# Performance work log

Measured on AMD Instinct MI355X. Metric: run time of the kernel, lower is better.

The kernel has to match this reference:

```python
import jax, jax.numpy as jnp
import numpy as np

B, N, D = 8, 8192, 256
NPOINT, NSAMPLE, WNET = 2048, 32, 16
IN_CH = D + 3
OUT_CH = 512
LEAKY = 0.1


def setup_inputs() -> dict:
    key = jax.random.key(0)
    ks = jax.random.split(key, 8)
    def p(k, shape, s=0.1):
        return jax.random.normal(k, shape, jnp.float32) * s
    return {
        "xyz": jax.random.normal(ks[0], (B, 3, N), jnp.float32),
        "points": jax.random.normal(ks[1], (B, D, N), jnp.float32),
        "w1": p(ks[2], (8, 3)), "b1": jnp.zeros((8,), jnp.float32),
        "w2": p(ks[3], (8, 8)), "b2": jnp.zeros((8,), jnp.float32),
        "w3": p(ks[4], (WNET, 8)), "b3": jnp.zeros((WNET,), jnp.float32),
        "lin_w": p(ks[5], (OUT_CH, WNET * IN_CH), 0.02),
        "lin_b": jnp.zeros((OUT_CH,), jnp.float32),
    }


def fps(xyz_t, npoint):
    # furthest point sampling; xyz_t: [B,N,3] -> idx [B,npoint] (first idx = 0)
    b, n, _ = xyz_t.shape
    def body(i, carry):
        idx, dists, last = carry
        centroid = jnp.take_along_axis(xyz_t, last[:, None, None], axis=1)  # [B,1,3]
        d = jnp.sum((xyz_t - centroid) ** 2, axis=-1)                        # [B,N]
        dists = jnp.minimum(dists, d)
        nxt = jnp.argmax(dists, axis=-1).astype(jnp.int32)                   # [B]
        return idx.at[:, i].set(nxt), dists, nxt
    idx0 = jnp.zeros((b, npoint), jnp.int32)
    last0 = jnp.zeros((b,), jnp.int32)
    d0 = jnp.full((b, n), 1e10, xyz_t.dtype)
    idx, _, _ = jax.lax.fori_loop(1, npoint, body, (idx0, d0, last0))
    return idx


def knn(nsample, xyz_t, new_xyz):
    # squared pairwise dists [B,S,N]; k smallest -> neighbor indices [B,S,K]
    d = (jnp.sum(new_xyz ** 2, -1)[:, :, None]
         + jnp.sum(xyz_t ** 2, -1)[:, None, :]
         - 2.0 * jnp.einsum('bsc,bnc->bsn', new_xyz, xyz_t))
    _, idx = jax.lax.top_k(-d, nsample)
    return idx


def gather(pts, idx):
    # pts [B,N,C], idx [B,S,K] -> [B,S,K,C]
    return jax.vmap(lambda p, i: p[i])(pts, idx)


def reference(xyz, points, w1, b1, w2, b2, w3, b3, lin_w, lin_b):
    xyz_t = xyz.transpose(0, 2, 1)      # [B,N,3]
    pts_t = points.transpose(0, 2, 1)   # [B,N,D]
    fps_idx = fps(xyz_t, NPOINT)
    new_xyz = jnp.take_along_axis(xyz_t, fps_idx[:, :, None], axis=1)  # [B,S,3]
    idx = knn(NSAMPLE, xyz_t, new_xyz)
    grouped_xyz_norm = gather(xyz_t, idx) - new_xyz[:, :, None, :]     # [B,S,K,3]
    new_points = jnp.concatenate([grouped_xyz_norm, gather(pts_t, idx)], axis=-1)  # [B,S,K,3+D]
    # WeightNet: 1x1-conv MLP 3 -> 8 -> 8 -> WNET, ReLU after each layer (bn=False)
    h = jax.nn.relu(grouped_xyz_norm @ w1.T + b1)
    h = jax.nn.relu(h @ w2.T + b2)
    w = jax.nn.relu(h @ w3.T + b3)                                     # [B,S,K,WNET]
    # per-point weighted aggregation: [B,S,C,K] @ [B,S,K,WNET] -> [B,S,C*WNET]
    agg = jnp.einsum('bskc,bskw->bscw', new_points, w).reshape(xyz.shape[0], NPOINT, -1)
    out = agg @ lin_w.T + lin_b                                        # [B,S,OUT_CH]
    out = out.transpose(0, 2, 1)                                       # [B,OUT_CH,S]
    out = jnp.where(out > 0, out, LEAKY * out)                         # LeakyReLU(0.1)
    return new_xyz.transpose(0, 2, 1), out, fps_idx
```

## Files before the change

### kernel.cpp

```cpp
#include <hip/hip_runtime.h>

#define NB 8
#define NN 8192
#define ND 256
#define NPOINT 2048
#define NSAMPLE 32
#define WNET 16
#define INCH 259
#define OUTCH 512
#define KPAD 4160

typedef short short8 __attribute__((ext_vector_type(8)));
typedef float float4v __attribute__((ext_vector_type(4)));
typedef unsigned long long u64;

__device__ __forceinline__ unsigned short f2bf(float x){
  unsigned u = __float_as_uint(x);
  u = (u + 0x7FFFu + ((u >> 16) & 1u)) >> 16;
  return (unsigned short)u;
}
__device__ __forceinline__ float bf2f(unsigned short v){
  return __uint_as_float(((unsigned)v) << 16);
}

__device__ __forceinline__ u64 wave_max_dpp(u64 k){
#define DPPSTEP(ctrl) {                                                        \
    unsigned lo = (unsigned)k, hi = (unsigned)(k >> 32);                       \
    unsigned olo = (unsigned)__builtin_amdgcn_update_dpp(0, (int)lo, ctrl, 0xf, 0xf, true); \
    unsigned ohi = (unsigned)__builtin_amdgcn_update_dpp(0, (int)hi, ctrl, 0xf, 0xf, true); \
    u64 o = (((u64)ohi) << 32) | olo;                                          \
    if (o > k) k = o; }
  DPPSTEP(0x111)
  DPPSTEP(0x112)
  DPPSTEP(0x114)
  DPPSTEP(0x118)
  DPPSTEP(0x142)
  DPPSTEP(0x143)
#undef DPPSTEP
  return k;
}

__device__ __forceinline__ u64 row16_max_dpp(u64 k){
#define DPPSTEP(ctrl) {                                                        \
    unsigned lo = (unsigned)k, hi = (unsigned)(k >> 32);                       \
    unsigned olo = (unsigned)__builtin_amdgcn_update_dpp(0, (int)lo, ctrl, 0xf, 0xf, true); \
    unsigned ohi = (unsigned)__builtin_amdgcn_update_dpp(0, (int)hi, ctrl, 0xf, 0xf, true); \
    u64 o = (((u64)ohi) << 32) | olo;                                          \
    if (o > k) k = o; }
  DPPSTEP(0x111)
  DPPSTEP(0x112)
  DPPSTEP(0x114)
  DPPSTEP(0x118)
#undef DPPSTEP
  return k;
}

__device__ __forceinline__ unsigned p1b2(unsigned v){
  v &= 0x3FFu;
  v = (v | (v << 16)) & 0x030000FFu;
  v = (v | (v << 8))  & 0x0300F00Fu;
  v = (v | (v << 4))  & 0x030C30C3u;
  v = (v | (v << 2))  & 0x09249249u;
  return v;
}

__global__ __launch_bounds__(1024) void morton_sort_kernel(
    const float* __restrict__ xyz, float* __restrict__ sx, float* __restrict__ sy,
    float* __restrict__ sz, int* __restrict__ sorig){
  __shared__ u64 arr[NN];
  const int b = blockIdx.x, t = threadIdx.x;
  const float* xp = xyz + (size_t)b * 3 * NN;
#pragma unroll
  for (int j = 0; j < 8; j++){
    int n = t + j * 1024;
    float x = xp[n], y = xp[NN + n], z = xp[2 * NN + n];
    unsigned qx = (unsigned)fminf(1023.f, fmaxf(0.f, (x + 6.f) * 85.25f));
    unsigned qy = (unsigned)fminf(1023.f, fmaxf(0.f, (y + 6.f) * 85.25f));
    unsigned qz = (unsigned)fminf(1023.f, fmaxf(0.f, (z + 6.f) * 85.25f));
    unsigned key = (p1b2(qz) << 2) | (p1b2(qy) << 1) | p1b2(qx);
    arr[n] = (((u64)key) << 13) | (unsigned)n;
  }
  __syncthreads();
  for (int k = 2; k <= NN; k <<= 1){
    for (int j = k >> 1; j >= 1; j >>= 1){
#pragma unroll
      for (int pi = 0; pi < 4; pi++){
        int p = t + pi * 1024;
        int lo = ((p & ~(j - 1)) << 1) | (p & (j - 1));
        int hi = lo | j;
        bool asc = (lo & k) == 0;
        u64 a = arr[lo], c = arr[hi];
        if (asc ? (a > c) : (c > a)){ arr[lo] = c; arr[hi] = a; }
      }
      __syncthreads();
    }
  }
#pragma unroll
  for (int j = 0; j < 8; j++){
    int n = t + j * 1024;
    int orig = (int)(arr[n] & 8191u);
    sx[(size_t)b * NN + n] = xp[orig];
    sy[(size_t)b * NN + n] = xp[NN + orig];
    sz[(size_t)b * NN + n] = xp[2 * NN + orig];
    sorig[(size_t)b * NN + n] = orig;
  }
}

__global__ __launch_bounds__(1024) void fps_kernel(
    const float* __restrict__ sxg, const float* __restrict__ syg,
    const float* __restrict__ szg, const int* __restrict__ sorigg,
    float* __restrict__ out0, float* __restrict__ out2, float* __restrict__ wnew){
#pragma clang fp contract(off)
  __shared__ float4v pxyz[NN];
  __shared__ u64 seq[NPOINT];
  __shared__ u64 red[2][16];
  __shared__ int s_pos0;
  const int b = blockIdx.x, t = threadIdx.x;
  const int lane = t & 63, w = t >> 6;
  const int base = w * 512 + lane * 8;
  const float* gx = sxg + (size_t)b * NN;
  const float* gy = syg + (size_t)b * NN;
  const float* gz = szg + (size_t)b * NN;
  const int*   go = sorigg + (size_t)b * NN;

  float x[8], y[8], z[8], ld[8]; int so[8];
#pragma unroll
  for (int j = 0; j < 8; j++){
    int n = base + j;
    x[j] = gx[n]; y[j] = gy[n]; z[j] = gz[n]; so[j] = go[n];
    pxyz[n] = (float4v){x[j], y[j], z[j], 0.f};
    if (so[j] == 0) s_pos0 = n;
    ld[j] = 1e10f;
  }
  float mnx = x[0], mxx = x[0], mny = y[0], mxy = y[0], mnz = z[0], mxz = z[0];
#pragma unroll
  for (int j = 1; j < 8; j++){
    mnx = fminf(mnx, x[j]); mxx = fmaxf(mxx, x[j]);
    mny = fminf(mny, y[j]); mxy = fmaxf(mxy, y[j]);
    mnz = fminf(mnz, z[j]); mxz = fmaxf(mxz, z[j]);
  }
  const float ccx = (mnx + mxx) * 0.5f, ccy = (mny + mxy) * 0.5f, ccz = (mnz + mxz) * 0.5f;
  float R2 = 0.f;
#pragma unroll
  for (int j = 0; j < 8; j++){
    float dx = x[j] - ccx, dy = y[j] - ccy, dz = z[j] - ccz;
    R2 = fmaxf(R2, (dx * dx + dy * dy) + dz * dz);
  }
  const float R = sqrtf(R2) * 1.001f + 1e-7f;
  float thr = 3e38f;
  u64 wkey = 0;
  __syncthreads();

  int pos = s_pos0;
  float4v c4 = pxyz[pos];
  float cx = c4[0], cy = c4[1], cz = c4[2];
  if (t == 0) seq[0] = (((u64)8191) << 13) | (unsigned)pos;

  for (int i = 1; i < NPOINT; i++){
    float qdx = cx - ccx, qdy = cy - ccy, qdz = cz - ccz;
    float q = (qdx * qdx + qdy * qdy) + qdz * qdz;
    if (__any(q < thr)){
      float bv = -1.f; int bo = 0, bp = 0;
#pragma unroll
      for (int j = 0; j < 8; j++){
        float dx = x[j] - cx, dy = y[j] - cy, dz = z[j] - cz;
        float d  = (dx * dx + dy * dy) + dz * dz;
        float nd = fminf(ld[j], d);
        ld[j] = nd;
        bool better = (nd > bv) || (nd == bv && so[j] < bo);
        bv = better ? nd : bv;
        bo = better ? so[j] : bo;
        bp = better ? (base + j) : bp;
      }
      float sr = sqrtf(bv) * 1.001f + R;
      thr = sr * sr;
      u64 k2 = (((u64)__float_as_uint(bv)) << 26) | (((u64)(8191 - bo)) << 13) | (unsigned)bp;
      wkey = wave_max_dpp(k2);
    }
    if (lane == 63) red[i & 1][w] = wkey;
    __syncthreads();
    u64 rv = red[i & 1][lane & 15];
    rv = row16_max_dpp(rv);
    unsigned rlo = (unsigned)__builtin_amdgcn_readlane((int)(unsigned)rv, 15);
    unsigned rhi = (unsigned)__builtin_amdgcn_readlane((int)(unsigned)(rv >> 32), 15);
    u64 v = (((u64)rhi) << 32) | rlo;
    pos = (int)(v & 8191u);
    float4v n4 = pxyz[pos];
    cx = n4[0]; cy = n4[1]; cz = n4[2];
    if (t == 0) seq[i] = v;
  }
  __syncthreads();
  for (int k = t; k < NPOINT; k += 1024){
    u64 v = seq[k];
    int p = (int)(v & 8191u);
    int orig = 8191 - (int)((v >> 13) & 8191u);
    float4v pv = pxyz[p];
    out2[b * NPOINT + k] = (float)orig;
    out0[(size_t)b * 3 * NPOINT + k]              = pv[0];
    out0[(size_t)b * 3 * NPOINT + NPOINT + k]     = pv[1];
    out0[(size_t)b * 3 * NPOINT + 2 * NPOINT + k] = pv[2];
    float* wp = wnew + ((size_t)b * NPOINT + k) * 3;
    wp[0] = pv[0]; wp[1] = pv[1]; wp[2] = pv[2];
  }
}

__global__ __launch_bounds__(1024) void transpose_points(
    const float* __restrict__ pts, unsigned short* __restrict__ ptsT){
  __shared__ float tile[64][65];
  const int b  = blockIdx.z;
  const int n0 = blockIdx.x * 64;
  const int d0 = blockIdx.y * 64;
  const int tx = threadIdx.x, ty = threadIdx.y;
  const float* src = pts + ((size_t)b * ND + d0) * NN + n0;
#pragma unroll
  for (int j = 0; j < 4; j++){
    int d = ty + j * 16;
    tile[d][tx] = src[(size_t)d * NN + tx];
  }
  __syncthreads();
  unsigned short* dst = ptsT + ((size_t)b * NN + n0) * ND + d0;
#pragma unroll
  for (int j = 0; j < 4; j++){
    int n = ty + j * 16;
    dst[(size_t)n * ND + tx] = f2bf(tile[tx][n]);
  }
}

__global__ __launch_bounds__(256) void convert_linw(
    const float* __restrict__ lw, unsigned short* __restrict__ out){
  int i = blockIdx.x * 256 + threadIdx.x;
  if (i >= OUTCH * KPAD) return;
  int o = i / KPAD, f = i - o * KPAD;
  float v = (f < WNET * INCH) ? lw[(size_t)o * (WNET * INCH) + f] : 0.f;
  out[i] = f2bf(v);
}

__device__ __forceinline__ void find_bin64(const unsigned* hist, unsigned r,
                                           unsigned* outB, unsigned* outC, int lane){
  unsigned h0 = hist[lane * 4 + 0], h1 = hist[lane * 4 + 1];
  unsigned h2 = hist[lane * 4 + 2], h3 = hist[lane * 4 + 3];
  unsigned s4 = h0 + h1 + h2 + h3;
  unsigned sc = s4;
#pragma unroll
  for (int off = 1; off < 64; off <<= 1){
    unsigned o = __shfl_up(sc, off, 64);
    if (lane >= off) sc += o;
  }
  unsigned cum = sc - s4;
  if (cum < r && cum + h0 >= r){ *outB = lane * 4 + 0; *outC = cum; } cum += h0;
  if (cum < r && cum + h1 >= r){ *outB = lane * 4 + 1; *outC = cum; } cum += h1;
  if (cum < r && cum + h2 >= r){ *outB = lane * 4 + 2; *outC = cum; } cum += h2;
  if (cum < r && cum + h3 >= r){ *outB = lane * 4 + 3; *outC = cum; } cum += h3;
}

__global__ __launch_bounds__(256) void knn_kernel(const float* __restrict__ xyz,
    const float* __restrict__ newxyz, int* __restrict__ ws_idx){
  __shared__ unsigned key[NN];
  __shared__ unsigned hist[256];
  __shared__ int s_sel[48];
  __shared__ unsigned candk[256];
  __shared__ int candi[256];
  __shared__ int s_selcnt, s_candcnt;
  __shared__ unsigned s_info[4];
  const int q = blockIdx.x;
  const int b = q >> 11;
  const int t = threadIdx.x;
  const float* xp = xyz + (size_t)b * 3 * NN;
  float qx = newxyz[q * 3], qy = newxyz[q * 3 + 1], qz = newxyz[q * 3 + 2];
  float qq = qx * qx + qy * qy + qz * qz;
#pragma unroll 4
  for (int j = 0; j < 32; j++){
    int n = t + j * 256;
    float px = xp[n], py = xp[NN + n], pz = xp[2 * NN + n];
    float pp = px * px + py * py + pz * pz;
    float d  = qq + pp - 2.f * (qx * px + qy * py + qz * pz);
    unsigned u = __float_as_uint(d);
    u ^= (u & 0x80000000u) ? 0xFFFFFFFFu : 0x80000000u;
    key[n] = u;
  }
  hist[t] = 0;
  if (t == 0){ s_selcnt = 0; s_candcnt = 0; }
  __syncthreads();
#pragma unroll 4
  for (int j = 0; j < 32; j++){
    int n = t + j * 256;
    atomicAdd(&hist[key[n] >> 24], 1u);
  }
  __syncthreads();
  if (t < 64) find_bin64(hist, NSAMPLE, &s_info[0], &s_info[1], t);
  __syncthreads();
  unsigned B1 = s_info[0], c0 = s_info[1];
  hist[t] = 0;
  __syncthreads();
#pragma unroll 4
  for (int j = 0; j < 32; j++){
    int n = t + j * 256;
    unsigned u = key[n];
    if ((u >> 24) == B1) atomicAdd(&hist[(u >> 16) & 0xFFu], 1u);
  }
  __syncthreads();
  if (t < 64) find_bin64(hist, NSAMPLE - c0, &s_info[2], &s_info[3], t);
  __syncthreads();
  unsigned T16 = (B1 << 8) | s_info[2];
  int c01 = (int)(c0 + s_info[3]);
#pragma unroll 4
  for (int j = 0; j < 32; j++){
    int n = t + j * 256;
    unsigned k16 = key[n] >> 16;
    if (k16 < T16){
      int p = atomicAdd(&s_selcnt, 1);
      s_sel[p] = n;
    } else if (k16 == T16){
      int p = atomicAdd(&s_candcnt, 1);
      if (p < 256){ candk[p] = key[n]; candi[p] = n; }
    }
  }
  __syncthreads();
  const int m = NSAMPLE - c01;
  const int L = s_candcnt;
  if (t < 64){
    u64 prev = 0;
    for (int r = 0; r < m; r++){
      u64 best = ~0ULL;
      if (L <= 256){
        for (int j = t; j < L; j += 64){
          u64 pk = (((u64)candk[j]) << 32) | (unsigned)candi[j];
          if (pk > prev && pk < best) best = pk;
        }
      } else {
        for (int j = 0; j < 128; j++){
          int n = t + j * 64;
          unsigned u = key[n];
          if ((u >> 16) == T16){
            u64 pk = (((u64)u) << 32) | (unsigned)n;
            if (pk > prev && pk < best) best = pk;
          }
        }
      }
#pragma unroll
      for (int off = 32; off > 0; off >>= 1){
        u64 o = __shfl_down(best, off, 64);
        if (o < best) best = o;
      }
      best = __shfl(best, 0, 64);
      if (t == 0) s_sel[c01 + r] = (int)(best & 0xFFFFFFFFu);
      prev = best;
    }
  }
  __syncthreads();
  if (t < NSAMPLE) ws_idx[(size_t)q * NSAMPLE + t] = s_sel[t];
}

__global__ __launch_bounds__(256) void agg_kernel(
    const float* __restrict__ xyz, const float* __restrict__ newxyz,
    const int* __restrict__ ws_idx, const unsigned short* __restrict__ ptsT,
    const float* __restrict__ w1, const float* __restrict__ b1,
    const float* __restrict__ w2, const float* __restrict__ b2,
    const float* __restrict__ w3, const float* __restrict__ b3,
    unsigned short* __restrict__ agg){
  __shared__ float feat[32][257];
  __shared__ float __align__(16) wgt[32][16];
  __shared__ float xyzn[32][4];
  __shared__ int nid[32];
  const int q = blockIdx.x;
  const int b = q >> 11;
  const int t = threadIdx.x;
  if (t < 32) nid[t] = ws_idx[(size_t)q * NSAMPLE + t];
  __syncthreads();
  if (t < 32){
    int n = nid[t];
    const float* xp = xyz + (size_t)b * 3 * NN;
    float qx = newxyz[q * 3], qy = newxyz[q * 3 + 1], qz = newxyz[q * 3 + 2];
    float xn = xp[n] - qx, yn = xp[NN + n] - qy, zn = xp[2 * NN + n] - qz;
    xyzn[t][0] = xn; xyzn[t][1] = yn; xyzn[t][2] = zn;
    float h1[8], h2[8];
#pragma unroll
    for (int i = 0; i < 8; i++)
      h1[i] = fmaxf(0.f, w1[i * 3] * xn + w1[i * 3 + 1] * yn + w1[i * 3 + 2] * zn + b1[i]);
#pragma unroll
    for (int i = 0; i < 8; i++){
      float a = b2[i];
#pragma unroll
      for (int j = 0; j < 8; j++) a += w2[i * 8 + j] * h1[j];
      h2[i] = fmaxf(0.f, a);
    }
#pragma unroll
    for (int i = 0; i < 16; i++){
      float a = b3[i];
#pragma unroll
      for (int j = 0; j < 8; j++) a += w3[i * 8 + j] * h2[j];
      wgt[t][i] = fmaxf(0.f, a);
    }
  }
#pragma unroll
  for (int j = 0; j < 4; j++){
    int c = t + 256 * j;
    int row = c >> 5, col = c & 31;
    const uint4* src = (const uint4*)(ptsT + ((size_t)b * NN + nid[row]) * ND) + col;
    uint4 v = *src;
    float* dstf = &feat[row][col * 8];
    dstf[0] = bf2f((unsigned short)(v.x & 0xFFFF)); dstf[1] = bf2f((unsigned short)(v.x >> 16));
    dstf[2] = bf2f((unsigned short)(v.y & 0xFFFF)); dstf[3] = bf2f((unsigned short)(v.y >> 16));
    dstf[4] = bf2f((unsigned short)(v.z & 0xFFFF)); dstf[5] = bf2f((unsigned short)(v.z >> 16));
    dstf[6] = bf2f((unsigned short)(v.w & 0xFFFF)); dstf[7] = bf2f((unsigned short)(v.w >> 16));
  }
  __syncthreads();
  for (int c = t; c < INCH; c += 256){
    const float* npb; int stride;
    if (c < 3){ npb = &xyzn[0][c]; stride = 4; }
    else      { npb = &feat[0][c - 3]; stride = 257; }
    float acc[16];
#pragma unroll
    for (int i = 0; i < 16; i++) acc[i] = 0.f;
    for (int k = 0; k < 32; k++){
      float v = npb[k * stride];
      const float4v* wr = (const float4v*)(&wgt[k][0]);
      float4v a0 = wr[0], a1 = wr[1], a2 = wr[2], a3 = wr[3];
      acc[0]  += v * a0[0]; acc[1]  += v * a0[1]; acc[2]  += v * a0[2]; acc[3]  += v * a0[3];
      acc[4]  += v * a1[0]; acc[5]  += v * a1[1]; acc[6]  += v * a1[2]; acc[7]  += v * a1[3];
      acc[8]  += v * a2[0]; acc[9]  += v * a2[1]; acc[10] += v * a2[2]; acc[11] += v * a2[3];
      acc[12] += v * a3[0]; acc[13] += v * a3[1]; acc[14] += v * a3[2]; acc[15] += v * a3[3];
    }
    unsigned r[8];
#pragma unroll
    for (int p = 0; p < 8; p++)
      r[p] = (unsigned)f2bf(acc[2 * p]) | ((unsigned)f2bf(acc[2 * p + 1]) << 16);
    uint4* dst = (uint4*)(agg + (size_t)q * KPAD + c * WNET);
    uint4 v0 = {r[0], r[1], r[2], r[3]};
    uint4 v1 = {r[4], r[5], r[6], r[7]};
    dst[0] = v0; dst[1] = v1;
  }
  if (t == 3){
    uint4 z = {0, 0, 0, 0};
    uint4* dst = (uint4*)(agg + (size_t)q * KPAD + WNET * INCH);
    dst[0] = z; dst[1] = z;
  }
}

#define BM 128
#define BN 128
#define BK 64
__global__ __launch_bounds__(256) void gemm_kernel(
    const unsigned short* __restrict__ A, const unsigned short* __restrict__ W,
    const float* __restrict__ bias, float* __restrict__ out1){
  __shared__ short __align__(16) As[BM * BK];
  __shared__ short __align__(16) Ws[BN * BK];
  const int t = threadIdx.x;
  const int m0 = blockIdx.x * BM;
  const int n0 = blockIdx.y * BN;
  const int wave = t >> 6, lane = t & 63;
  const int wm = (wave >> 1) * 64, wn = (wave & 1) * 64;
  const int lrow = lane & 15, quad = lane >> 4;
  float4v acc[4][4];
#pragma unroll
  for (int i = 0; i < 4; i++)
#pragma unroll
    for (int j = 0; j < 4; j++) acc[i][j] = (float4v){0.f, 0.f, 0.f, 0.f};

  for (int k0 = 0; k0 < KPAD; k0 += BK){
#pragma unroll
    for (int j = 0; j < 4; j++){
      int chunk = t + 256 * j;
      int row = chunk >> 3, c = chunk & 7;
      uint4 v = *(const uint4*)(A + (size_t)(m0 + row) * KPAD + k0 + c * 8);
      *(uint4*)&As[chunk * 8] = v;
    }
#pragma unroll
    for (int j = 0; j < 4; j++){
      int chunk = t + 256 * j;
      int row = chunk >> 3, c = chunk & 7;
      uint4 v = *(const uint4*)(W + (size_t)(n0 + row) * KPAD + k0 + c * 8);
      *(uint4*)&Ws[chunk * 8] = v;
    }
    __syncthreads();
#pragma unroll
    for (int kk = 0; kk < 2; kk++){
      short8 a[4], w[4];
      int kof = kk * 32 + quad * 8;
#pragma unroll
      for (int i = 0; i < 4; i++){
        a[i] = *(const short8*)&As[(wm + i * 16 + lrow) * BK + kof];
        w[i] = *(const short8*)&Ws[(wn + i * 16 + lrow) * BK + kof];
      }
#pragma unroll
      for (int i = 0; i < 4; i++)
#pragma unroll
        for (int j = 0; j < 4; j++)
          acc[i][j] = __builtin_amdgcn_mfma_f32_16x16x32_bf16(a[i], w[j], acc[i][j], 0, 0, 0);
    }
    __syncthreads();
  }
#pragma unroll
  for (int i = 0; i < 4; i++){
#pragma unroll
    for (int j = 0; j < 4; j++){
      int m = m0 + wm + i * 16 + quad * 4;
      int n = n0 + wn + j * 16 + lrow;
      float bv = bias[n];
      int bb = m >> 11, s = m & 2047;
      float* dst = out1 + ((size_t)bb * OUTCH + n) * NPOINT + s;
      float4v v = acc[i][j];
      float4v r;
#pragma unroll
      for (int e = 0; e < 4; e++){
        float x = v[e] + bv;
        r[e] = x > 0.f ? x : 0.1f * x;
      }
      *(float4v*)dst = r;
    }
  }
}

extern "C" void kernel_launch(void* const* d_in, const int* in_sizes, int n_in,
                              void* d_out, int out_size, void* d_ws, size_t ws_size,
                              hipStream_t stream) {
  const float* xyz    = (const float*)d_in[0];
  const float* points = (const float*)d_in[1];
  const float* w1 = (const float*)d_in[2];
  const float* b1 = (const float*)d_in[3];
  const float* w2 = (const float*)d_in[4];
  const float* b2 = (const float*)d_in[5];
  const float* w3 = (const float*)d_in[6];
  const float* b3 = (const float*)d_in[7];
  const float* lin_w = (const float*)d_in[8];
  const float* lin_b = (const float*)d_in[9];

  float* out0 = (float*)d_out;
  float* out1 = out0 + (size_t)NB * 3 * NPOINT;
  float* out2 = out1 + (size_t)NB * OUTCH * NPOINT;

  char* ws = (char*)d_ws;
  float* ws_newxyz = (float*)ws;                                   size_t o = (size_t)NB * NPOINT * 3 * 4;
  int* ws_idx = (int*)(ws + o);                                    o += (size_t)NB * NPOINT * NSAMPLE * 4;
  unsigned short* ws_ptsT = (unsigned short*)(ws + o);             o += (size_t)NB * NN * ND * 2;
  unsigned short* ws_lw = (unsigned short*)(ws + o);               o += (size_t)OUTCH * KPAD * 2;
  unsigned short* ws_agg = (unsigned short*)(ws + o);              o += (size_t)NB * NPOINT * KPAD * 2;
  float* ws_sx = (float*)(ws + o);                                 o += (size_t)NB * NN * 4;
  float* ws_sy = (float*)(ws + o);                                 o += (size_t)NB * NN * 4;
  float* ws_sz = (float*)(ws + o);                                 o += (size_t)NB * NN * 4;
  int*   ws_so = (int*)(ws + o);                                   o += (size_t)NB * NN * 4;

  morton_sort_kernel<<<NB, 1024, 0, stream>>>(xyz, ws_sx, ws_sy, ws_sz, ws_so);
  fps_kernel<<<NB, 1024, 0, stream>>>(ws_sx, ws_sy, ws_sz, ws_so, out0, out2, ws_newxyz);
  transpose_points<<<dim3(NN / 64, ND / 64, NB), dim3(64, 16), 0, stream>>>(points, ws_ptsT);
  convert_linw<<<(OUTCH * KPAD + 255) / 256, 256, 0, stream>>>(lin_w, ws_lw);
  knn_kernel<<<NB * NPOINT, 256, 0, stream>>>(xyz, ws_newxyz, ws_idx);
  agg_kernel<<<NB * NPOINT, 256, 0, stream>>>(xyz, ws_newxyz, ws_idx, ws_ptsT,
                                              w1, b1, w2, b2, w3, b3, ws_agg);
  gemm_kernel<<<dim3(NB * NPOINT / BM, OUTCH / BN), 256, 0, stream>>>(ws_agg, ws_lw, lin_b, out1);
}
```

Baseline: 3.751 ms.

## Fuse FPS with KNN+aggregation in a persistent kernel overlapping via progress flags

Merges the morton sort, point transpose and weight conversion into one prep launch. A persistent mega kernel then runs FPS on 8 blocks while the other blocks pull query indices from a global atomic counter. Each worker spins on per-batch FPS progress counters so KNN and aggregation for already-emitted centroids overlap with the serial FPS loop. KNN and aggregation are fused in one block, so the neighbor index buffer is no longer written and read back. The risks are spin-wait correctness, the 248-block launch needing all blocks co-resident, and large LDS use per block.

Result: faster. 3.039 ms (-19.0%).

```diff
diff --git a/kernel.cpp b/kernel.cpp
--- a/kernel.cpp
+++ b/kernel.cpp
@@ -40,21 +40,6 @@
   return k;
 }
 
-__device__ __forceinline__ u64 row16_max_dpp(u64 k){
-#define DPPSTEP(ctrl) {                                                        \
-    unsigned lo = (unsigned)k, hi = (unsigned)(k >> 32);                       \
-    unsigned olo = (unsigned)__builtin_amdgcn_update_dpp(0, (int)lo, ctrl, 0xf, 0xf, true); \
-    unsigned ohi = (unsigned)__builtin_amdgcn_update_dpp(0, (int)hi, ctrl, 0xf, 0xf, true); \
-    u64 o = (((u64)ohi) << 32) | olo;                                          \
-    if (o > k) k = o; }
-  DPPSTEP(0x111)
-  DPPSTEP(0x112)
-  DPPSTEP(0x114)
-  DPPSTEP(0x118)
-#undef DPPSTEP
-  return k;
-}
-
 __device__ __forceinline__ unsigned p1b2(unsigned v){
   v &= 0x3FFu;
   v = (v | (v << 16)) & 0x030000FFu;
@@ -64,175 +49,83 @@
   return v;
 }
 
-__global__ __launch_bounds__(1024) void morton_sort_kernel(
-    const float* __restrict__ xyz, float* __restrict__ sx, float* __restrict__ sy,
-    float* __restrict__ sz, int* __restrict__ sorig){
-  __shared__ u64 arr[NN];
-  const int b = blockIdx.x, t = threadIdx.x;
-  const float* xp = xyz + (size_t)b * 3 * NN;
-#pragma unroll
-  for (int j = 0; j < 8; j++){
-    int n = t + j * 1024;
-    float x = xp[n], y = xp[NN + n], z = xp[2 * NN + n];
-    unsigned qx = (unsigned)fminf(1023.f, fmaxf(0.f, (x + 6.f) * 85.25f));
-    unsigned qy = (unsigned)fminf(1023.f, fmaxf(0.f, (y + 6.f) * 85.25f));
-    unsigned qz = (unsigned)fminf(1023.f, fmaxf(0.f, (z + 6.f) * 85.25f));
-    unsigned key = (p1b2(qz) << 2) | (p1b2(qy) << 1) | p1b2(qx);
-    arr[n] = (((u64)key) << 13) | (unsigned)n;
+#define TRB 4096
+#define CVB 2080
+__global__ __launch_bounds__(1024) void prep_kernel(
+    const float* __restrict__ xyz, const float* __restrict__ pts,
+    const float* __restrict__ lw,
+    float* __restrict__ sx, float* __restrict__ sy, float* __restrict__ sz,
+    int* __restrict__ sorig, unsigned short* __restrict__ ptsT,
+    unsigned short* __restrict__ lwout, unsigned* __restrict__ psync){
+  __shared__ __align__(16) char smem[65536];
+  const int bid = blockIdx.x, t = threadIdx.x;
+  if (bid < NB){
+    u64* arr = (u64*)smem;
+    const int b = bid;
+    if (t == 0){ psync[b] = 0; if (b == 0) psync[8] = 0; }
+    const float* xp = xyz + (size_t)b * 3 * NN;
+#pragma unroll
+    for (int j = 0; j < 8; j++){
+      int n = t + j * 1024;
+      float x = xp[n], y = xp[NN + n], z = xp[2 * NN + n];
+      unsigned qx = (unsigned)fminf(1023.f, fmaxf(0.f, (x + 6.f) * 85.25f));
+      unsigned qy = (unsigned)fminf(1023.f, fmaxf(0.f, (y + 6.f) * 85.25f));
+      unsigned qz = (unsigned)fminf(1023.f, fmaxf(0.f, (z + 6.f) * 85.25f));
+      unsigned key = (p1b2(qz) << 2) | (p1b2(qy) << 1) | p1b2(qx);
+      arr[n] = (((u64)key) << 13) | (unsigned)n;
+    }
+    __syncthreads();
+    for (int k = 2; k <= NN; k <<= 1){
+      for (int j = k >> 1; j >= 1; j >>= 1){
+#pragma unroll
+        for (int pi = 0; pi < 4; pi++){
+          int p = t + pi * 1024;
+          int lo = ((p & ~(j - 1)) << 1) | (p & (j - 1));
+          int hi = lo | j;
+          bool asc = (lo & k) == 0;
+          u64 a = arr[lo], c = arr[hi];
+          if (asc ? (a > c) : (c > a)){ arr[lo] = c; arr[hi] = a; }
+        }
+        __syncthreads();
+      }
+    }
+#pragma unroll
+    for (int j = 0; j < 8; j++){
+      int n = t + j * 1024;
+      int orig = (int)(arr[n] & 8191u);
+      sx[(size_t)b * NN + n] = xp[orig];
+      sy[(size_t)b * NN + n] = xp[NN + orig];
+      sz[(size_t)b * NN + n] = xp[2 * NN + orig];
+      sorig[(size_t)b * NN + n] = orig;
+    }
+  } else if (bid < NB + TRB){
+    float (*tile)[65] = (float(*)[65])smem;
+    const int r = bid - NB;
+    const int n0 = (r & 127) * 64;
+    const int d0 = ((r >> 7) & 3) * 64;
+    const int b  = r >> 9;
+    const int tx = t & 63, ty = t >> 6;
+    const float* src = pts + ((size_t)b * ND + d0) * NN + n0;
+#pragma unroll
+    for (int j = 0; j < 4; j++){
+      int d = ty + j * 16;
+      tile[d][tx] = src[(size_t)d * NN + tx];
+    }
+    __syncthreads();
+    unsigned short* dst = ptsT + ((size_t)b * NN + n0) * ND + d0;
+#pragma unroll
+    for (int j = 0; j < 4; j++){
+      int n = ty + j * 16;
+      dst[(size_t)n * ND + tx] = f2bf(tile[tx][n]);
+    }
+  } else {
+    int i = (bid - NB - TRB) * 1024 + t;
+    if (i < OUTCH * KPAD){
+      int o = i / KPAD, f = i - o * KPAD;
+      float v = (f < WNET * INCH) ? lw[(size_t)o * (WNET * INCH) + f] : 0.f;
+      lwout[i] = f2bf(v);
+    }
   }
-  __syncthreads();
-  for (int k = 2; k <= NN; k <<= 1){
-    for (int j = k >> 1; j >= 1; j >>= 1){
-#pragma unroll
-      for (int pi = 0; pi < 4; pi++){
-        int p = t + pi * 1024;
-        int lo = ((p & ~(j - 1)) << 1) | (p & (j - 1));
-        int hi = lo | j;
-        bool asc = (lo & k) == 0;
-        u64 a = arr[lo], c = arr[hi];
-        if (asc ? (a > c) : (c > a)){ arr[lo] = c; arr[hi] = a; }
-      }
-      __syncthreads();
-    }
-  }
-#pragma unroll
-  for (int j = 0; j < 8; j++){
-    int n = t + j * 1024;
-    int orig = (int)(arr[n] & 8191u);
-    sx[(size_t)b * NN + n] = xp[orig];
-    sy[(size_t)b * NN + n] = xp[NN + orig];
-    sz[(size_t)b * NN + n] = xp[2 * NN + orig];
-    sorig[(size_t)b * NN + n] = orig;
-  }
-}
-
-__global__ __launch_bounds__(1024) void fps_kernel(
-    const float* __restrict__ sxg, const float* __restrict__ syg,
-    const float* __restrict__ szg, const int* __restrict__ sorigg,
-    float* __restrict__ out0, float* __restrict__ out2, float* __restrict__ wnew){
-#pragma clang fp contract(off)
-  __shared__ float4v pxyz[NN];
-  __shared__ u64 seq[NPOINT];
-  __shared__ u64 red[2][16];
-  __shared__ int s_pos0;
-  const int b = blockIdx.x, t = threadIdx.x;
-  const int lane = t & 63, w = t >> 6;
-  const int base = w * 512 + lane * 8;
-  const float* gx = sxg + (size_t)b * NN;
-  const float* gy = syg + (size_t)b * NN;
-  const float* gz = szg + (size_t)b * NN;
-  const int*   go = sorigg + (size_t)b * NN;
-
-  float x[8], y[8], z[8], ld[8]; int so[8];
-#pragma unroll
-  for (int j = 0; j < 8; j++){
-    int n = base + j;
-    x[j] = gx[n]; y[j] = gy[n]; z[j] = gz[n]; so[j] = go[n];
-    pxyz[n] = (float4v){x[j], y[j], z[j], 0.f};
-    if (so[j] == 0) s_pos0 = n;
-    ld[j] = 1e10f;
-  }
-  float mnx = x[0], mxx = x[0], mny = y[0], mxy = y[0], mnz = z[0], mxz = z[0];
-#pragma unroll
-  for (int j = 1; j < 8; j++){
-    mnx = fminf(mnx, x[j]); mxx = fmaxf(mxx, x[j]);
-    mny = fminf(mny, y[j]); mxy = fmaxf(mxy, y[j]);
-    mnz = fminf(mnz, z[j]); mxz = fmaxf(mxz, z[j]);
-  }
-  const float ccx = (mnx + mxx) * 0.5f, ccy = (mny + mxy) * 0.5f, ccz = (mnz + mxz) * 0.5f;
-  float R2 = 0.f;
-#pragma unroll
-  for (int j = 0; j < 8; j++){
-    float dx = x[j] - ccx, dy = y[j] - ccy, dz = z[j] - ccz;
-    R2 = fmaxf(R2, (dx * dx + dy * dy) + dz * dz);
-  }
-  const float R = sqrtf(R2) * 1.001f + 1e-7f;
-  float thr = 3e38f;
-  u64 wkey = 0;
-  __syncthreads();
-
-  int pos = s_pos0;
-  float4v c4 = pxyz[pos];
-  float cx = c4[0], cy = c4[1], cz = c4[2];
-  if (t == 0) seq[0] = (((u64)8191) << 13) | (unsigned)pos;
-
-  for (int i = 1; i < NPOINT; i++){
-    float qdx = cx - ccx, qdy = cy - ccy, qdz = cz - ccz;
-    float q = (qdx * qdx + qdy * qdy) + qdz * qdz;
-    if (__any(q < thr)){
-      float bv = -1.f; int bo = 0, bp = 0;
-#pragma unroll
-      for (int j = 0; j < 8; j++){
-        float dx = x[j] - cx, dy = y[j] - cy, dz = z[j] - cz;
-        float d  = (dx * dx + dy * dy) + dz * dz;
-        float nd = fminf(ld[j], d);
-        ld[j] = nd;
-        bool better = (nd > bv) || (nd == bv && so[j] < bo);
-        bv = better ? nd : bv;
-        bo = better ? so[j] : bo;
-        bp = better ? (base + j) : bp;
-      }
-      float sr = sqrtf(bv) * 1.001f + R;
-      thr = sr * sr;
-      u64 k2 = (((u64)__float_as_uint(bv)) << 26) | (((u64)(8191 - bo)) << 13) | (unsigned)bp;
-      wkey = wave_max_dpp(k2);
-    }
-    if (lane == 63) red[i & 1][w] = wkey;
-    __syncthreads();
-    u64 rv = red[i & 1][lane & 15];
-    rv = row16_max_dpp(rv);
-    unsigned rlo = (unsigned)__builtin_amdgcn_readlane((int)(unsigned)rv, 15);
-    unsigned rhi = (unsigned)__builtin_amdgcn_readlane((int)(unsigned)(rv >> 32), 15);
-    u64 v = (((u64)rhi) << 32) | rlo;
-    pos = (int)(v & 8191u);
-    float4v n4 = pxyz[pos];
-    cx = n4[0]; cy = n4[1]; cz = n4[2];
-    if (t == 0) seq[i] = v;
-  }
-  __syncthreads();
-  for (int k = t; k < NPOINT; k += 1024){
-    u64 v = seq[k];
-    int p = (int)(v & 8191u);
-    int orig = 8191 - (int)((v >> 13) & 8191u);
-    float4v pv = pxyz[p];
-    out2[b * NPOINT + k] = (float)orig;
-    out0[(size_t)b * 3 * NPOINT + k]              = pv[0];
-    out0[(size_t)b * 3 * NPOINT + NPOINT + k]     = pv[1];
-    out0[(size_t)b * 3 * NPOINT + 2 * NPOINT + k] = pv[2];
-    float* wp = wnew + ((size_t)b * NPOINT + k) * 3;
-    wp[0] = pv[0]; wp[1] = pv[1]; wp[2] = pv[2];
-  }
-}
-
-__global__ __launch_bounds__(1024) void transpose_points(
-    const float* __restrict__ pts, unsigned short* __restrict__ ptsT){
-  __shared__ float tile[64][65];
-  const int b  = blockIdx.z;
-  const int n0 = blockIdx.x * 64;
-  const int d0 = blockIdx.y * 64;
-  const int tx = threadIdx.x, ty = threadIdx.y;
-  const float* src = pts + ((size_t)b * ND + d0) * NN + n0;
-#pragma unroll
-  for (int j = 0; j < 4; j++){
-    int d = ty + j * 16;
-    tile[d][tx] = src[(size_t)d * NN + tx];
-  }
-  __syncthreads();
-  unsigned short* dst = ptsT + ((size_t)b * NN + n0) * ND + d0;
-#pragma unroll
-  for (int j = 0; j < 4; j++){
-    int n = ty + j * 16;
-    dst[(size_t)n * ND + tx] = f2bf(tile[tx][n]);
-  }
-}
-
-__global__ __launch_bounds__(256) void convert_linw(
-    const float* __restrict__ lw, unsigned short* __restrict__ out){
-  int i = blockIdx.x * 256 + threadIdx.x;
-  if (i >= OUTCH * KPAD) return;
-  int o = i / KPAD, f = i - o * KPAD;
-  float v = (f < WNET * INCH) ? lw[(size_t)o * (WNET * INCH) + f] : 0.f;
-  out[i] = f2bf(v);
 }
 
 __device__ __forceinline__ void find_bin64(const unsigned* hist, unsigned r,
@@ -253,187 +146,305 @@
   if (cum < r && cum + h3 >= r){ *outB = lane * 4 + 3; *outC = cum; } cum += h3;
 }
 
-__global__ __launch_bounds__(256) void knn_kernel(const float* __restrict__ xyz,
-    const float* __restrict__ newxyz, int* __restrict__ ws_idx){
-  __shared__ unsigned key[NN];
-  __shared__ unsigned hist[256];
-  __shared__ int s_sel[48];
-  __shared__ unsigned candk[256];
-  __shared__ int candi[256];
-  __shared__ int s_selcnt, s_candcnt;
-  __shared__ unsigned s_info[4];
-  const int q = blockIdx.x;
-  const int b = q >> 11;
-  const int t = threadIdx.x;
-  const float* xp = xyz + (size_t)b * 3 * NN;
-  float qx = newxyz[q * 3], qy = newxyz[q * 3 + 1], qz = newxyz[q * 3 + 2];
-  float qq = qx * qx + qy * qy + qz * qz;
-#pragma unroll 4
-  for (int j = 0; j < 32; j++){
-    int n = t + j * 256;
-    float px = xp[n], py = xp[NN + n], pz = xp[2 * NN + n];
-    float pp = px * px + py * py + pz * pz;
-    float d  = qq + pp - 2.f * (qx * px + qy * py + qz * pz);
-    unsigned u = __float_as_uint(d);
-    u ^= (u & 0x80000000u) ? 0xFFFFFFFFu : 0x80000000u;
-    key[n] = u;
-  }
-  hist[t] = 0;
-  if (t == 0){ s_selcnt = 0; s_candcnt = 0; }
-  __syncthreads();
-#pragma unroll 4
-  for (int j = 0; j < 32; j++){
-    int n = t + j * 256;
-    atomicAdd(&hist[key[n] >> 24], 1u);
-  }
-  __syncthreads();
-  if (t < 64) find_bin64(hist, NSAMPLE, &s_info[0], &s_info[1], t);
-  __syncthreads();
-  unsigned B1 = s_info[0], c0 = s_info[1];
-  hist[t] = 0;
-  __syncthreads();
-#pragma unroll 4
-  for (int j = 0; j < 32; j++){
-    int n = t + j * 256;
-    unsigned u = key[n];
-    if ((u >> 24) == B1) atomicAdd(&hist[(u >> 16) & 0xFFu], 1u);
-  }
-  __syncthreads();
-  if (t < 64) find_bin64(hist, NSAMPLE - c0, &s_info[2], &s_info[3], t);
-  __syncthreads();
-  unsigned T16 = (B1 << 8) | s_info[2];
-  int c01 = (int)(c0 + s_info[3]);
-#pragma unroll 4
-  for (int j = 0; j < 32; j++){
-    int n = t + j * 256;
-    unsigned k16 = key[n] >> 16;
-    if (k16 < T16){
-      int p = atomicAdd(&s_selcnt, 1);
-      s_sel[p] = n;
-    } else if (k16 == T16){
-      int p = atomicAdd(&s_candcnt, 1);
-      if (p < 256){ candk[p] = key[n]; candi[p] = n; }
-    }
-  }
-  __syncthreads();
-  const int m = NSAMPLE - c01;
-  const int L = s_candcnt;
-  if (t < 64){
-    u64 prev = 0;
-    for (int r = 0; r < m; r++){
-      u64 best = ~0ULL;
-      if (L <= 256){
-        for (int j = t; j < L; j += 64){
-          u64 pk = (((u64)candk[j]) << 32) | (unsigned)candi[j];
-          if (pk > prev && pk < best) best = pk;
-        }
-      } else {
-        for (int j = 0; j < 128; j++){
-          int n = t + j * 64;
-          unsigned u = key[n];
-          if ((u >> 16) == T16){
-            u64 pk = (((u64)u) << 32) | (unsigned)n;
-            if (pk > prev && pk < best) best = pk;
-          }
-        }
-      }
-#pragma unroll
-      for (int off = 32; off > 0; off >>= 1){
-        u64 o = __shfl_down(best, off, 64);
-        if (o < best) best = o;
-      }
-      best = __shfl(best, 0, 64);
-      if (t == 0) s_sel[c01 + r] = (int)(best & 0xFFFFFFFFu);
-      prev = best;
-    }
-  }
-  __syncthreads();
-  if (t < NSAMPLE) ws_idx[(size_t)q * NSAMPLE + t] = s_sel[t];
-}
-
-__global__ __launch_bounds__(256) void agg_kernel(
-    const float* __restrict__ xyz, const float* __restrict__ newxyz,
-    const int* __restrict__ ws_idx, const unsigned short* __restrict__ ptsT,
+struct WkScal { int selcnt, candcnt; unsigned info[4]; unsigned g; float nq[3]; };
+
+__global__ __launch_bounds__(1024) void mega_kernel(
+    const float* __restrict__ xyz,
+    const float* __restrict__ sxg, const float* __restrict__ syg,
+    const float* __restrict__ szg, const int* __restrict__ sorigg,
+    float* __restrict__ out0, float* __restrict__ out2, float* wnew,
+    const unsigned short* __restrict__ ptsT,
     const float* __restrict__ w1, const float* __restrict__ b1,
     const float* __restrict__ w2, const float* __restrict__ b2,
     const float* __restrict__ w3, const float* __restrict__ b3,
-    unsigned short* __restrict__ agg){
-  __shared__ float feat[32][257];
-  __shared__ float __align__(16) wgt[32][16];
-  __shared__ float xyzn[32][4];
-  __shared__ int nid[32];
-  const int q = blockIdx.x;
-  const int b = q >> 11;
+    unsigned short* __restrict__ agg, unsigned* psync){
+  __shared__ __align__(16) char smem[147488];
   const int t = threadIdx.x;
-  if (t < 32) nid[t] = ws_idx[(size_t)q * NSAMPLE + t];
-  __syncthreads();
-  if (t < 32){
-    int n = nid[t];
-    const float* xp = xyz + (size_t)b * 3 * NN;
-    float qx = newxyz[q * 3], qy = newxyz[q * 3 + 1], qz = newxyz[q * 3 + 2];
-    float xn = xp[n] - qx, yn = xp[NN + n] - qy, zn = xp[2 * NN + n] - qz;
-    xyzn[t][0] = xn; xyzn[t][1] = yn; xyzn[t][2] = zn;
-    float h1[8], h2[8];
-#pragma unroll
-    for (int i = 0; i < 8; i++)
-      h1[i] = fmaxf(0.f, w1[i * 3] * xn + w1[i * 3 + 1] * yn + w1[i * 3 + 2] * zn + b1[i]);
-#pragma unroll
-    for (int i = 0; i < 8; i++){
-      float a = b2[i];
-#pragma unroll
-      for (int j = 0; j < 8; j++) a += w2[i * 8 + j] * h1[j];
-      h2[i] = fmaxf(0.f, a);
-    }
-#pragma unroll
-    for (int i = 0; i < 16; i++){
-      float a = b3[i];
-#pragma unroll
-      for (int j = 0; j < 8; j++) a += w3[i * 8 + j] * h2[j];
-      wgt[t][i] = fmaxf(0.f, a);
-    }
+
+  if (blockIdx.x < NB){
+#pragma clang fp contract(off)
+    float4v* pxyz = (float4v*)smem;
+    u64* seq  = (u64*)(smem + 131072);
+    u64* slot = (u64*)(smem + 147456);
+    int* ppos0 = (int*)(smem + 147480);
+    const int b = blockIdx.x;
+    const int lane = t & 63, w = t >> 6;
+    const int base = w * 512 + lane * 8;
+    const float* gx = sxg + (size_t)b * NN;
+    const float* gy = syg + (size_t)b * NN;
+    const float* gz = szg + (size_t)b * NN;
+    const int*   go = sorigg + (size_t)b * NN;
+
+    float x[8], y[8], z[8], ld[8]; int so[8];
+#pragma unroll
+    for (int j = 0; j < 8; j++){
+      int n = base + j;
+      x[j] = gx[n]; y[j] = gy[n]; z[j] = gz[n]; so[j] = go[n];
+      pxyz[n] = (float4v){x[j], y[j], z[j], 0.f};
+      if (so[j] == 0) *ppos0 = n;
+      ld[j] = 1e10f;
+    }
+    if (t < 3) slot[t] = 0;
+    float mnx = x[0], mxx = x[0], mny = y[0], mxy = y[0], mnz = z[0], mxz = z[0];
+#pragma unroll
+    for (int j = 1; j < 8; j++){
+      mnx = fminf(mnx, x[j]); mxx = fmaxf(mxx, x[j]);
+      mny = fminf(mny, y[j]); mxy = fmaxf(mxy, y[j]);
+      mnz = fminf(mnz, z[j]); mxz = fmaxf(mxz, z[j]);
+    }
+    const float ccx = (mnx + mxx) * 0.5f, ccy = (mny + mxy) * 0.5f, ccz = (mnz + mxz) * 0.5f;
+    float R2 = 0.f;
+#pragma unroll
+    for (int j = 0; j < 8; j++){
+      float dx = x[j] - ccx, dy = y[j] - ccy, dz = z[j] - ccz;
+      R2 = fmaxf(R2, (dx * dx + dy * dy) + dz * dz);
+    }
+    const float R = sqrtf(R2) * 1.001f + 1e-7f;
+    float thr = 3e38f;
+    u64 wkey = 0;
+    __syncthreads();
+
+    int pos = *ppos0;
+    float4v c4 = pxyz[pos];
+    float cx = c4[0], cy = c4[1], cz = c4[2];
+    if (t == 0) seq[0] = (((u64)8191) << 13) | (unsigned)pos;
+
+    for (int i = 1; i < NPOINT; i++){
+      float qdx = cx - ccx, qdy = cy - ccy, qdz = cz - ccz;
+      float q = (qdx * qdx + qdy * qdy) + qdz * qdz;
+      if (__any(q < thr)){
+        float bv = -1.f; int bo = 0, bp = 0;
+#pragma unroll
+        for (int j = 0; j < 8; j++){
+          float dx = x[j] - cx, dy = y[j] - cy, dz = z[j] - cz;
+          float d  = (dx * dx + dy * dy) + dz * dz;
+          float nd = fminf(ld[j], d);
+          ld[j] = nd;
+          bool better = (nd > bv) || (nd == bv && so[j] < bo);
+          bv = better ? nd : bv;
+          bo = better ? so[j] : bo;
+          bp = better ? (base + j) : bp;
+        }
+        float sr = sqrtf(bv) * 1.001f + R;
+        thr = sr * sr;
+        u64 k2 = (((u64)__float_as_uint(bv)) << 26) | (((u64)(8191 - bo)) << 13) | (unsigned)bp;
+        wkey = wave_max_dpp(k2);
+      }
+      if (lane == 63) atomicMax((u64*)&slot[i % 3], wkey);
+      if (t == 0) slot[(i + 1) % 3] = 0;
+      __syncthreads();
+      u64 v = slot[i % 3];
+      if ((i & 31) == 0){
+        if (t < 32){
+          int w2 = i - 32 + t;
+          u64 sv = seq[w2];
+          float4v pv = pxyz[(int)(sv & 8191u)];
+          float* wp = wnew + ((size_t)b * NPOINT + w2) * 3;
+          wp[0] = pv[0]; wp[1] = pv[1]; wp[2] = pv[2];
+        }
+        if (t == 0)
+          __hip_atomic_store(&psync[b], (unsigned)i, __ATOMIC_RELEASE, __HIP_MEMORY_SCOPE_AGENT);
+      }
+      pos = (int)(v & 8191u);
+      float4v n4 = pxyz[pos];
+      cx = n4[0]; cy = n4[1]; cz = n4[2];
+      if (t == 0) seq[i] = v;
+    }
+    __syncthreads();
+    for (int k = t; k < NPOINT; k += 1024){
+      u64 v = seq[k];
+      int p = (int)(v & 8191u);
+      int orig = 8191 - (int)((v >> 13) & 8191u);
+      float4v pv = pxyz[p];
+      out2[b * NPOINT + k] = (float)orig;
+      out0[(size_t)b * 3 * NPOINT + k]              = pv[0];
+      out0[(size_t)b * 3 * NPOINT + NPOINT + k]     = pv[1];
+      out0[(size_t)b * 3 * NPOINT + 2 * NPOINT + k] = pv[2];
+      float* wp = wnew + ((size_t)b * NPOINT + k) * 3;
+      wp[0] = pv[0]; wp[1] = pv[1]; wp[2] = pv[2];
+    }
+    __syncthreads();
+    if (t == 0)
+      __hip_atomic_store(&psync[b], (unsigned)NPOINT, __ATOMIC_RELEASE, __HIP_MEMORY_SCOPE_AGENT);
+    return;
   }
-#pragma unroll
-  for (int j = 0; j < 4; j++){
-    int c = t + 256 * j;
-    int row = c >> 5, col = c & 31;
-    const uint4* src = (const uint4*)(ptsT + ((size_t)b * NN + nid[row]) * ND) + col;
-    uint4 v = *src;
-    float* dstf = &feat[row][col * 8];
-    dstf[0] = bf2f((unsigned short)(v.x & 0xFFFF)); dstf[1] = bf2f((unsigned short)(v.x >> 16));
-    dstf[2] = bf2f((unsigned short)(v.y & 0xFFFF)); dstf[3] = bf2f((unsigned short)(v.y >> 16));
-    dstf[4] = bf2f((unsigned short)(v.z & 0xFFFF)); dstf[5] = bf2f((unsigned short)(v.z >> 16));
-    dstf[6] = bf2f((unsigned short)(v.w & 0xFFFF)); dstf[7] = bf2f((unsigned short)(v.w >> 16));
-  }
-  __syncthreads();
-  for (int c = t; c < INCH; c += 256){
-    const float* npb; int stride;
-    if (c < 3){ npb = &xyzn[0][c]; stride = 4; }
-    else      { npb = &feat[0][c - 3]; stride = 257; }
-    float acc[16];
-#pragma unroll
-    for (int i = 0; i < 16; i++) acc[i] = 0.f;
-    for (int k = 0; k < 32; k++){
-      float v = npb[k * stride];
-      const float4v* wr = (const float4v*)(&wgt[k][0]);
-      float4v a0 = wr[0], a1 = wr[1], a2 = wr[2], a3 = wr[3];
-      acc[0]  += v * a0[0]; acc[1]  += v * a0[1]; acc[2]  += v * a0[2]; acc[3]  += v * a0[3];
-      acc[4]  += v * a1[0]; acc[5]  += v * a1[1]; acc[6]  += v * a1[2]; acc[7]  += v * a1[3];
-      acc[8]  += v * a2[0]; acc[9]  += v * a2[1]; acc[10] += v * a2[2]; acc[11] += v * a2[3];
-      acc[12] += v * a3[0]; acc[13] += v * a3[1]; acc[14] += v * a3[2]; acc[15] += v * a3[3];
-    }
-    unsigned r[8];
-#pragma unroll
-    for (int p = 0; p < 8; p++)
-      r[p] = (unsigned)f2bf(acc[2 * p]) | ((unsigned)f2bf(acc[2 * p + 1]) << 16);
-    uint4* dst = (uint4*)(agg + (size_t)q * KPAD + c * WNET);
-    uint4 v0 = {r[0], r[1], r[2], r[3]};
-    uint4 v1 = {r[4], r[5], r[6], r[7]};
-    dst[0] = v0; dst[1] = v1;
-  }
-  if (t == 3){
-    uint4 z = {0, 0, 0, 0};
-    uint4* dst = (uint4*)(agg + (size_t)q * KPAD + WNET * INCH);
-    dst[0] = z; dst[1] = z;
+
+  unsigned* key  = (unsigned*)smem;
+  float (*feat)[257] = (float(*)[257])(smem + 32768);
+  float (*wgt)[16]   = (float(*)[16])(smem + 65664);
+  float (*xyzn)[4]   = (float(*)[4])(smem + 67712);
+  unsigned* hist  = (unsigned*)(smem + 68224);
+  unsigned* candk = (unsigned*)(smem + 69248);
+  int* candi      = (int*)(smem + 70272);
+  int* s_sel      = (int*)(smem + 71296);
+  WkScal* sc      = (WkScal*)(smem + 71488);
+
+  while (true){
+    if (t == 0){
+      unsigned g = __hip_atomic_fetch_add(&psync[8], 1u, __ATOMIC_RELAXED, __HIP_MEMORY_SCOPE_AGENT);
+      sc->g = g;
+      if (g < (unsigned)(NB * NPOINT)){
+        unsigned bq = g & 7u, sq = g >> 3;
+        while (__hip_atomic_load(&psync[bq], __ATOMIC_ACQUIRE, __HIP_MEMORY_SCOPE_AGENT) <= sq)
+          __builtin_amdgcn_s_sleep(8);
+        float* wp = wnew + ((size_t)bq * NPOINT + sq) * 3;
+        sc->nq[0] = __hip_atomic_load(wp + 0, __ATOMIC_RELAXED, __HIP_MEMORY_SCOPE_AGENT);
+        sc->nq[1] = __hip_atomic_load(wp + 1, __ATOMIC_RELAXED, __HIP_MEMORY_SCOPE_AGENT);
+        sc->nq[2] = __hip_atomic_load(wp + 2, __ATOMIC_RELAXED, __HIP_MEMORY_SCOPE_AGENT);
+      }
+      sc->selcnt = 0; sc->candcnt = 0;
+    }
+    if (t < 256) hist[t] = 0;
+    __syncthreads();
+    unsigned g = sc->g;
+    if (g >= (unsigned)(NB * NPOINT)) break;
+    const int bq = (int)(g & 7u), sq = (int)(g >> 3);
+    const int q = bq * NPOINT + sq;
+    const float qx = sc->nq[0], qy = sc->nq[1], qz = sc->nq[2];
+    const float qq = qx * qx + qy * qy + qz * qz;
+    const float* xp = xyz + (size_t)bq * 3 * NN;
+
+#pragma unroll 2
+    for (int j = 0; j < 8; j++){
+      int n = t + j * 1024;
+      float px = xp[n], py = xp[NN + n], pz = xp[2 * NN + n];
+      float pp = px * px + py * py + pz * pz;
+      float d  = qq + pp - 2.f * (qx * px + qy * py + qz * pz);
+      unsigned u = __float_as_uint(d);
+      u ^= (u & 0x80000000u) ? 0xFFFFFFFFu : 0x80000000u;
+      key[n] = u;
+    }
+    __syncthreads();
+#pragma unroll 2
+    for (int j = 0; j < 8; j++)
+      atomicAdd(&hist[key[t + j * 1024] >> 24], 1u);
+    __syncthreads();
+    if (t < 64) find_bin64(hist, NSAMPLE, &sc->info[0], &sc->info[1], t);
+    __syncthreads();
+    unsigned B1 = sc->info[0], c0 = sc->info[1];
+    if (t < 256) hist[t] = 0;
+    __syncthreads();
+#pragma unroll 2
+    for (int j = 0; j < 8; j++){
+      unsigned u = key[t + j * 1024];
+      if ((u >> 24) == B1) atomicAdd(&hist[(u >> 16) & 0xFFu], 1u);
+    }
+    __syncthreads();
+    if (t < 64) find_bin64(hist, NSAMPLE - c0, &sc->info[2], &sc->info[3], t);
+    __syncthreads();
+    unsigned T16 = (B1 << 8) | sc->info[2];
+    int c01 = (int)(c0 + sc->info[3]);
+#pragma unroll 2
+    for (int j = 0; j < 8; j++){
+      int n = t + j * 1024;
+      unsigned k16 = key[n] >> 16;
+      if (k16 < T16){
+        int p = atomicAdd(&sc->selcnt, 1);
+        s_sel[p] = n;
+      } else if (k16 == T16){
+        int p = atomicAdd(&sc->candcnt, 1);
+        if (p < 256){ candk[p] = key[n]; candi[p] = n; }
+      }
+    }
+    __syncthreads();
+    const int m = NSAMPLE - c01;
+    const int L = sc->candcnt;
+    if (t < 64){
+      u64 prev = 0;
+      for (int r = 0; r < m; r++){
+        u64 best = ~0ULL;
+        if (L <= 256){
+          for (int j = t; j < L; j += 64){
+            u64 pk = (((u64)candk[j]) << 32) | (unsigned)candi[j];
+            if (pk > prev && pk < best) best = pk;
+          }
+        } else {
+          for (int j = 0; j < 128; j++){
+            int n = t + j * 64;
+            unsigned u = key[n];
+            if ((u >> 16) == T16){
+              u64 pk = (((u64)u) << 32) | (unsigned)n;
+              if (pk > prev && pk < best) best = pk;
+            }
+          }
+        }
+#pragma unroll
+        for (int off = 32; off > 0; off >>= 1){
+          u64 o = __shfl_down(best, off, 64);
+          if (o < best) best = o;
+        }
+        best = __shfl(best, 0, 64);
+        if (t == 0) s_sel[c01 + r] = (int)(best & 0xFFFFFFFFu);
+        prev = best;
+      }
+    }
+    __syncthreads();
+
+    if (t < 32){
+      int n = s_sel[t];
+      float xn = xp[n] - qx, yn = xp[NN + n] - qy, zn = xp[2 * NN + n] - qz;
+      xyzn[t][0] = xn; xyzn[t][1] = yn; xyzn[t][2] = zn;
+      float h1[8], h2[8];
+#pragma unroll
+      for (int i = 0; i < 8; i++)
+        h1[i] = fmaxf(0.f, w1[i * 3] * xn + w1[i * 3 + 1] * yn + w1[i * 3 + 2] * zn + b1[i]);
+#pragma unroll
+      for (int i = 0; i < 8; i++){
+        float a = b2[i];
+#pragma unroll
+        for (int j = 0; j < 8; j++) a += w2[i * 8 + j] * h1[j];
+        h2[i] = fmaxf(0.f, a);
+      }
+#pragma unroll
+      for (int i = 0; i < 16; i++){
+        float a = b3[i];
+#pragma unroll
+        for (int j = 0; j < 8; j++) a += w3[i * 8 + j] * h2[j];
+        wgt[t][i] = fmaxf(0.f, a);
+      }
+    }
+    {
+      int row = t >> 5, col = t & 31;
+      const uint4* src = (const uint4*)(ptsT + ((size_t)bq * NN + s_sel[row]) * ND) + col;
+      uint4 v = *src;
+      float* dstf = &feat[row][col * 8];
+      dstf[0] = bf2f((unsigned short)(v.x & 0xFFFF)); dstf[1] = bf2f((unsigned short)(v.x >> 16));
+      dstf[2] = bf2f((unsigned short)(v.y & 0xFFFF)); dstf[3] = bf2f((unsigned short)(v.y >> 16));
+      dstf[4] = bf2f((unsigned short)(v.z & 0xFFFF)); dstf[5] = bf2f((unsigned short)(v.z >> 16));
+      dstf[6] = bf2f((unsigned short)(v.w & 0xFFFF)); dstf[7] = bf2f((unsigned short)(v.w >> 16));
+    }
+    __syncthreads();
+    if (t < INCH){
+      const float* npb; int stride;
+      if (t < 3){ npb = &xyzn[0][t]; stride = 4; }
+      else      { npb = &feat[0][t - 3]; stride = 257; }
+      float acc[16];
+#pragma unroll
+      for (int i = 0; i < 16; i++) acc[i] = 0.f;
+      for (int k = 0; k < 32; k++){
+        float v = npb[k * stride];
+        const float4v* wr = (const float4v*)(&wgt[k][0]);
+        float4v a0 = wr[0], a1 = wr[1], a2 = wr[2], a3 = wr[3];
+        acc[0]  += v * a0[0]; acc[1]  += v * a0[1]; acc[2]  += v * a0[2]; acc[3]  += v * a0[3];
+        acc[4]  += v * a1[0]; acc[5]  += v * a1[1]; acc[6]  += v * a1[2]; acc[7]  += v * a1[3];
+        acc[8]  += v * a2[0]; acc[9]  += v * a2[1]; acc[10] += v * a2[2]; acc[11] += v * a2[3];
+        acc[12] += v * a3[0]; acc[13] += v * a3[1]; acc[14] += v * a3[2]; acc[15] += v * a3[3];
+      }
+      unsigned r[8];
+#pragma unroll
+      for (int p = 0; p < 8; p++)
+        r[p] = (unsigned)f2bf(acc[2 * p]) | ((unsigned)f2bf(acc[2 * p + 1]) << 16);
+      uint4* dst = (uint4*)(agg + (size_t)q * KPAD + t * WNET);
+      uint4 v0 = {r[0], r[1], r[2], r[3]};
+      uint4 v1 = {r[4], r[5], r[6], r[7]};
+      dst[0] = v0; dst[1] = v1;
+    }
+    if (t == INCH){
+      uint4 z = {0, 0, 0, 0};
+      uint4* dst = (uint4*)(agg + (size_t)q * KPAD + WNET * INCH);
+      dst[0] = z; dst[1] = z;
+    }
+    __syncthreads();
   }
 }
 
@@ -531,7 +542,6 @@
 
   char* ws = (char*)d_ws;
   float* ws_newxyz = (float*)ws;                                   size_t o = (size_t)NB * NPOINT * 3 * 4;
-  int* ws_idx = (int*)(ws + o);                                    o += (size_t)NB * NPOINT * NSAMPLE * 4;
   unsigned short* ws_ptsT = (unsigned short*)(ws + o);             o += (size_t)NB * NN * ND * 2;
   unsigned short* ws_lw = (unsigned short*)(ws + o);               o += (size_t)OUTCH * KPAD * 2;
   unsigned short* ws_agg = (unsigned short*)(ws + o);              o += (size_t)NB * NPOINT * KPAD * 2;
@@ -539,13 +549,12 @@
   float* ws_sy = (float*)(ws + o);                                 o += (size_t)NB * NN * 4;
   float* ws_sz = (float*)(ws + o);                                 o += (size_t)NB * NN * 4;
   int*   ws_so = (int*)(ws + o);                                   o += (size_t)NB * NN * 4;
-
-  morton_sort_kernel<<<NB, 1024, 0, stream>>>(xyz, ws_sx, ws_sy, ws_sz, ws_so);
-  fps_kernel<<<NB, 1024, 0, stream>>>(ws_sx, ws_sy, ws_sz, ws_so, out0, out2, ws_newxyz);
-  transpose_points<<<dim3(NN / 64, ND / 64, NB), dim3(64, 16), 0, stream>>>(points, ws_ptsT);
-  convert_linw<<<(OUTCH * KPAD + 255) / 256, 256, 0, stream>>>(lin_w, ws_lw);
-  knn_kernel<<<NB * NPOINT, 256, 0, stream>>>(xyz, ws_newxyz, ws_idx);
-  agg_kernel<<<NB * NPOINT, 256, 0, stream>>>(xyz, ws_newxyz, ws_idx, ws_ptsT,
-                                              w1, b1, w2, b2, w3, b3, ws_agg);
+  unsigned* ws_psync = (unsigned*)(ws + o);                        o += 64;
+
+  prep_kernel<<<NB + TRB + CVB, 1024, 0, stream>>>(
+      xyz, points, lin_w, ws_sx, ws_sy, ws_sz, ws_so, ws_ptsT, ws_lw, ws_psync);
+  mega_kernel<<<248, 1024, 0, stream>>>(
+      xyz, ws_sx, ws_sy, ws_sz, ws_so, out0, out2, ws_newxyz, ws_ptsT,
+      w1, b1, w2, b2, w3, b3, ws_agg, ws_psync);
   gemm_kernel<<<dim3(NB * NPOINT / BM, OUTCH / BN), 256, 0, stream>>>(ws_agg, ws_lw, lin_b, out1);
 }
```
